# Kernel tuning notes

Measured on AMD Instinct MI355X. Metric: run time of the kernel, lower is better.

## Reference

```python
import jax, jax.numpy as jnp
import numpy as np

NF = 64   # num_feat
DG = 8    # deformable_groups (also conv groups)
B, H, W = 4, 96, 96
K = 9     # 3x3 kernel positions


def _conv(x, w, b, padding=1, dilation=1, groups=1):
    out = jax.lax.conv_general_dilated(
        x, w, (1, 1), [(padding, padding), (padding, padding)],
        rhs_dilation=(dilation, dilation),
        dimension_numbers=('NCHW', 'OIHW', 'NCHW'),
        feature_group_count=groups)
    return out + b[None, :, None, None]


def _lrelu(t):
    return jnp.where(t >= 0, t, 0.1 * t)


def _cat_align(a, b):
    # channel-interleaved concat: [a0,b0,a1,b1,...]
    Bn, k, h, w = a.shape
    return jnp.stack([a, b], axis=2).reshape(Bn, 2 * k, h, w)


def _deform_conv(x, offset, mask, weight, bias, dilation, padding):
    # DCNv2 modulated deformable conv, stride 1.
    Bn, C, h, w = x.shape
    Cpg = C // DG
    off = offset.reshape(Bn, DG, K, 2, h, w)          # (dy, dx) per group/kernel pos
    m = mask.reshape(Bn, DG, K, h, w)
    ky = (jnp.repeat(jnp.arange(3), 3) * dilation - padding).astype(x.dtype)  # (K,)
    kx = (jnp.tile(jnp.arange(3), 3) * dilation - padding).astype(x.dtype)
    hs = jnp.arange(h, dtype=x.dtype)
    ws = jnp.arange(w, dtype=x.dtype)
    py = off[:, :, :, 0] + ky[None, None, :, None, None] + hs[None, None, None, :, None]
    px = off[:, :, :, 1] + kx[None, None, :, None, None] + ws[None, None, None, None, :]
    y0f = jnp.floor(py); x0f = jnp.floor(px)
    ly = (py - y0f)[:, :, None]  # broadcast over Cpg
    lx = (px - x0f)[:, :, None]
    y0 = y0f.astype(jnp.int32); x0 = x0f.astype(jnp.int32)
    xg = x.reshape(Bn, DG, Cpg, h * w)

    def gather(yi, xi):
        inb = ((yi >= 0) & (yi < h) & (xi >= 0) & (xi < w))
        idx = (jnp.clip(yi, 0, h - 1) * w + jnp.clip(xi, 0, w - 1)).reshape(Bn, DG, 1, K * h * w)
        v = jnp.take_along_axis(xg, jnp.broadcast_to(idx, (Bn, DG, Cpg, K * h * w)), axis=3)
        return v.reshape(Bn, DG, Cpg, K, h, w) * inb[:, :, None].astype(x.dtype)

    v00 = gather(y0, x0); v01 = gather(y0, x0 + 1)
    v10 = gather(y0 + 1, x0); v11 = gather(y0 + 1, x0 + 1)
    val = (v00 * (1 - ly) * (1 - lx) + v01 * (1 - ly) * lx
           + v10 * ly * (1 - lx) + v11 * ly * lx) * m[:, :, None]
    sampled = val.reshape(Bn, C, K, h, w)
    out = jnp.einsum('bckhw,ock->bohw', sampled, weight.reshape(weight.shape[0], C, K))
    return out + bias[None, :, None, None]


def _dcn(x, off_feat, om_w, om_b, w, b, dilation):
    pad = dilation  # int(3/2)*dilation
    out = _conv(off_feat, om_w, om_b, padding=pad, dilation=dilation)
    o1, o2, msk = jnp.split(out, 3, axis=1)
    offset = jnp.concatenate([o1, o2], axis=1)
    mask = jax.nn.sigmoid(msk)
    return _deform_conv(x, offset, mask, w, b, dilation, pad)


def setup_inputs() -> dict:
    key = jax.random.key(0)
    ks = iter(jax.random.split(key, 64))
    def rn(shape, s=0.05):
        return jax.random.normal(next(ks), shape, jnp.float32) * s
    d = {}
    d['nbr_feat'] = jax.random.normal(next(ks), (B, NF, H, W), jnp.float32)
    d['ref_feat'] = jax.random.normal(next(ks), (B, NF, H, W), jnp.float32)
    for lv, has3 in [('l3', False), ('l2', True), ('l1', True)]:
        d[f'oc1_w_{lv}'] = rn((NF, 2 * NF // DG, 3, 3)); d[f'oc1_b_{lv}'] = rn((NF,))
        oc2_in = 2 * NF if has3 else NF
        d[f'oc2_w_{lv}'] = rn((NF, oc2_in // DG, 3, 3)); d[f'oc2_b_{lv}'] = rn((NF,))
        if has3:
            d[f'oc3_w_{lv}'] = rn((NF, NF // DG, 3, 3)); d[f'oc3_b_{lv}'] = rn((NF,))
            d[f'fc_w_{lv}'] = rn((NF, 2 * NF // DG, 3, 3)); d[f'fc_b_{lv}'] = rn((NF,))
        d[f'om_w_{lv}'] = rn((DG * 3 * K, NF, 3, 3), 0.01); d[f'om_b_{lv}'] = rn((DG * 3 * K,), 0.01)
        d[f'dcn_w_{lv}'] = rn((NF, NF, 3, 3)); d[f'dcn_b_{lv}'] = rn((NF,))
    d['cas_oc1_w'] = rn((NF, 2 * NF // DG, 3, 3)); d['cas_oc1_b'] = rn((NF,))
    d['cas_oc2_w'] = rn((NF, NF // DG, 3, 3)); d['cas_oc2_b'] = rn((NF,))
    d['cas_om_w'] = rn((DG * 3 * K, NF, 3, 3), 0.01); d['cas_om_b'] = rn((DG * 3 * K,), 0.01)
    d['cas_w'] = rn((NF, NF, 3, 3)); d['cas_b'] = rn((NF,))
    return d


def reference(nbr_feat, ref_feat,
              oc1_w_l3, oc1_b_l3, oc2_w_l3, oc2_b_l3, om_w_l3, om_b_l3, dcn_w_l3, dcn_b_l3,
              oc1_w_l2, oc1_b_l2, oc2_w_l2, oc2_b_l2, oc3_w_l2, oc3_b_l2, fc_w_l2, fc_b_l2,
              om_w_l2, om_b_l2, dcn_w_l2, dcn_b_l2,
              oc1_w_l1, oc1_b_l1, oc2_w_l1, oc2_b_l1, oc3_w_l1, oc3_b_l1, fc_w_l1, fc_b_l1,
              om_w_l1, om_b_l1, dcn_w_l1, dcn_b_l1,
              cas_oc1_w, cas_oc1_b, cas_oc2_w, cas_oc2_b, cas_om_w, cas_om_b, cas_w, cas_b):
    # level 3 (dilation 5)
    off = _lrelu(_conv(_cat_align(nbr_feat, ref_feat), oc1_w_l3, oc1_b_l3, groups=DG))
    off = _lrelu(_conv(off, oc2_w_l3, oc2_b_l3, groups=DG))
    feat = _lrelu(_dcn(nbr_feat, off, om_w_l3, om_b_l3, dcn_w_l3, dcn_b_l3, 5))
    to, tf = off, feat
    # level 2 (dilation 3)
    off = _lrelu(_conv(_cat_align(nbr_feat, ref_feat), oc1_w_l2, oc1_b_l2, groups=DG))
    off = _lrelu(_conv(_cat_align(off, to), oc2_w_l2, oc2_b_l2, groups=DG))
    off = _lrelu(_conv(off, oc3_w_l2, oc3_b_l2, groups=DG))
    feat = _dcn(nbr_feat, off, om_w_l2, om_b_l2, dcn_w_l2, dcn_b_l2, 3)
    feat = _lrelu(_conv(_cat_align(feat, tf), fc_w_l2, fc_b_l2, groups=DG))
    to, tf = off, feat
    # level 1 (dilation 1), no lrelu on feat
    off = _lrelu(_conv(_cat_align(nbr_feat, ref_feat), oc1_w_l1, oc1_b_l1, groups=DG))
    off = _lrelu(_conv(_cat_align(off, to), oc2_w_l1, oc2_b_l1, groups=DG))
    off = _lrelu(_conv(off, oc3_w_l1, oc3_b_l1, groups=DG))
    feat = _dcn(nbr_feat, off, om_w_l1, om_b_l1, dcn_w_l1, dcn_b_l1, 1)
    feat = _conv(_cat_align(feat, tf), fc_w_l1, fc_b_l1, groups=DG)
    # cascade
    off = _cat_align(feat, ref_feat)
    off = _lrelu(_conv(_lrelu(_conv(off, cas_oc1_w, cas_oc1_b, groups=DG)), cas_oc2_w, cas_oc2_b, groups=DG))
    feat = _lrelu(_dcn(feat, off, cas_om_w, cas_om_b, cas_w, cas_b, 1))
    return feat
```

## Files before the change

### kernel.cpp

```cpp
#include <hip/hip_runtime.h>

#define BATCH 4
#define NFEAT 64
#define DGRP 8
#define HH 96
#define WW 96
#define HWP (HH*WW)

typedef short short4a __attribute__((ext_vector_type(4)));
typedef short short8 __attribute__((ext_vector_type(8)));
typedef float f32x4 __attribute__((ext_vector_type(4)));
typedef float f32x16 __attribute__((ext_vector_type(16)));

__device__ inline short f2bf(float f) {
  union { float f; unsigned u; } v; v.f = f;
  unsigned r = v.u + 0x7fff + ((v.u >> 16) & 1);
  return (short)(r >> 16);
}
__device__ inline float bf2f(short s) {
  return __uint_as_float(((unsigned)(unsigned short)s) << 16);
}

__global__ __launch_bounds__(256) void prep_om(
    const float* __restrict__ s0, const float* __restrict__ s1,
    const float* __restrict__ s2, const float* __restrict__ s3,
    short* __restrict__ dst) {
  int gid = blockIdx.x * 256 + threadIdx.x;
  if (gid >= 4 * 147456) return;
  int t = gid / 147456, r = gid % 147456;
  int tile = r / 18432, r2 = r % 18432;
  int kk = r2 / 512, r3 = r2 % 512;
  int lane = r3 / 8, j = r3 % 8;
  int col = lane & 31, half = lane >> 5;
  int oc = tile * 32 + col;
  int k = kk * 16 + half * 8 + j;
  int p = k >> 6, c = k & 63;
  const float* s = (t == 0) ? s0 : (t == 1) ? s1 : (t == 2) ? s2 : s3;
  float v = (oc < 216) ? s[(size_t)oc * 576 + c * 9 + p] : 0.f;
  dst[gid] = f2bf(v);
}

__global__ __launch_bounds__(256) void prep_dcnw(
    const float* __restrict__ s0, const float* __restrict__ s1,
    const float* __restrict__ s2, const float* __restrict__ s3,
    short* __restrict__ dst) {
  int gid = blockIdx.x * 256 + threadIdx.x;
  if (gid >= 4 * 36864) return;
  int t = gid / 36864, r = gid % 36864;
  int tile = r / 18432, r2 = r % 18432;
  int kk = r2 / 512, r3 = r2 % 512;
  int lane = r3 / 8, j = r3 % 8;
  int col = lane & 31, half = lane >> 5;
  int oc = tile * 32 + col;
  int k = kk * 16 + half * 8 + j;
  int p = k >> 6, c = k & 63;
  const float* s = (t == 0) ? s0 : (t == 1) ? s1 : (t == 2) ? s2 : s3;
  dst[gid] = f2bf(s[(size_t)oc * 576 + c * 9 + p]);
}

struct GwArgs {
  const float* src[12];
  int cat[12];
  int base[13];
};

__global__ __launch_bounds__(256) void prep_gw(GwArgs a, short* __restrict__ dst) {
  int gid = blockIdx.x * 256 + threadIdx.x;
  if (gid >= a.base[12]) return;
  int t = 0;
  while (gid >= a.base[t + 1]) ++t;
  int r = gid - a.base[t];
  const float* s = a.src[t];
  const int tsz = a.cat[t] ? 4608 : 2560;
  int tile = r / tsz, r2 = r % tsz;
  int kk = r2 / 512, r3 = r2 % 512;
  int lane = r3 >> 3, j = r3 & 7;
  int m = lane & 15, quad = lane >> 4;
  int oc = tile * 16 + m;
  int j32 = quad * 8 + j;
  float val = 0.f;
  if (a.cat[t]) {
    int gsel = j32 >> 4, ssel = (j32 >> 3) & 1, ch8 = j32 & 7;
    if (gsel == (m >> 3)) val = s[oc * 144 + (2 * ch8 + ssel) * 9 + kk];
  } else {
    int tapsel = j32 >> 4, gsel = (j32 >> 3) & 1, ch8 = j32 & 7;
    int p = 2 * kk + tapsel;
    if (p < 9 && gsel == (m >> 3)) val = s[oc * 72 + ch8 * 9 + p];
  }
  dst[gid] = f2bf(val);
}

__global__ __launch_bounds__(256) void transpose_bf16(
    const float* __restrict__ in0, short* __restrict__ out0,
    const float* __restrict__ in1, short* __restrict__ out1) {
  const float* in = blockIdx.z ? in1 : in0;
  short* out = blockIdx.z ? out1 : out0;
  __shared__ float s[64][65];
  const int p0 = blockIdx.x * 64;
  const int b = blockIdx.y;
  const int tx = threadIdx.x, ty = threadIdx.y;
  for (int c = ty; c < 64; c += 4)
    s[c][tx] = in[((size_t)b * NFEAT + c) * HWP + p0 + tx];
  __syncthreads();
  for (int p = ty; p < 64; p += 4)
    out[((size_t)b * HWP + p0 + p) * NFEAT + tx] = f2bf(s[tx][p]);
}

template <bool CAT, bool LRELU>
__device__ __forceinline__ void gconv_body(
    const short* __restrict__ in0, const short* __restrict__ in1,
    const short* __restrict__ Wsh, const float* __restrict__ bias,
    short* __restrict__ out, int pixbase, int b) {
  const int lane = threadIdx.x, t = threadIdx.y;
  const int n = lane & 15, quad = lane >> 4;
  constexpr int NKK = CAT ? 9 : 5;

  short8 A[NKK];
#pragma unroll
  for (int kk = 0; kk < NKK; ++kk)
    A[kk] = *(const short8*)(Wsh + ((size_t)(t * NKK + kk) * 64 + lane) * 8);

  const short* sb;
  if (CAT) {
    sb = ((quad & 1) ? in1 : in0) + (size_t)b * HWP * 64 + (2 * t + (quad >> 1)) * 8;
  } else {
    sb = in0 + (size_t)b * HWP * 64 + (2 * t + (quad & 1)) * 8;
  }

  f32x4 acc[2] = {};
#pragma unroll
  for (int nt = 0; nt < 2; ++nt) {
    const int pix = pixbase + nt * 16 + n;
    const int yp = pix / WW, xp = pix % WW;
#pragma unroll
    for (int kk = 0; kk < NKK; ++kk) {
      const int p = CAT ? kk : (2 * kk + (quad >> 1));
      short8 B = {0, 0, 0, 0, 0, 0, 0, 0};
      if (p < 9) {
        const int sy = yp + p / 3 - 1, sx = xp + p % 3 - 1;
        if (((unsigned)sy < (unsigned)HH) && ((unsigned)sx < (unsigned)WW))
          B = *(const short8*)(sb + (size_t)(sy * WW + sx) * 64);
      }
      acc[nt] = __builtin_amdgcn_mfma_f32_16x16x32_bf16(A[kk], B, acc[nt], 0, 0, 0);
    }
  }

  const int ocb = t * 16 + quad * 4;
  const float b0 = bias[ocb], b1 = bias[ocb + 1], b2 = bias[ocb + 2], b3 = bias[ocb + 3];
#pragma unroll
  for (int nt = 0; nt < 2; ++nt) {
    float v0 = acc[nt][0] + b0, v1 = acc[nt][1] + b1;
    float v2 = acc[nt][2] + b2, v3 = acc[nt][3] + b3;
    if (LRELU) {
      v0 = (v0 >= 0.f) ? v0 : 0.1f * v0;
      v1 = (v1 >= 0.f) ? v1 : 0.1f * v1;
      v2 = (v2 >= 0.f) ? v2 : 0.1f * v2;
      v3 = (v3 >= 0.f) ? v3 : 0.1f * v3;
    }
    short4a pk = {f2bf(v0), f2bf(v1), f2bf(v2), f2bf(v3)};
    *(short4a*)(out + ((size_t)b * HWP + pixbase + nt * 16 + n) * 64 + ocb) = pk;
  }
}

template <bool CAT, bool LRELU>
__global__ __launch_bounds__(256) void gconv_mfma(
    const short* __restrict__ in0, const short* __restrict__ in1,
    const short* __restrict__ Wsh, const float* __restrict__ bias,
    short* __restrict__ out) {
  gconv_body<CAT, LRELU>(in0, in1, Wsh, bias, out, blockIdx.x * 32, blockIdx.y);
}

struct Oc1Args {
  const short* W[3];
  const float* bias[3];
  short* out[3];
};

__global__ __launch_bounds__(256) void gconv_oc1x3(
    const short* __restrict__ in0, const short* __restrict__ in1, Oc1Args a) {
  const int job = blockIdx.z;
  gconv_body<true, true>(in0, in1, a.W[job], a.bias[job], a.out[job],
                         blockIdx.x * 32, blockIdx.y);
}

#define OMPITCH 580
#define OMLP 33

template <int D, bool LRELU, bool PMOUT>
__global__ __launch_bounds__(256) void omdcn_fused(
    const short* __restrict__ omIn,
    const short* __restrict__ xT,
    const short* __restrict__ Wom,
    const float* __restrict__ obias,
    const short* __restrict__ Wd,
    const float* __restrict__ bias,
    void* __restrict__ outv) {
  __shared__ __align__(16) char smem[37120 + 14256];
  short* Bs = (short*)smem;
  short* Ls = (short*)smem;
  short* om_lds = (short*)(smem + 37120);
  float* red = (float*)(smem + 37120);

  const int tx = threadIdx.x, ty = threadIdx.y;
  const int lid = ty * 32 + tx;
  const int lane = lid & 63, w = lid >> 6;
  const int col = lane & 31, half = lane >> 5;
  const int pb = blockIdx.x, b = blockIdx.y;
  const int pixbase = pb * 32;

  {
    const short* pixb = omIn + (size_t)b * HWP * 64;
#pragma unroll
    for (int t = 0; t < 9; ++t) {
      const int i = lid + t * 256;
      const int row = i / 72, q = i % 72;
      const int p = q >> 3, c8 = q & 7;
      const int pix = pixbase + row;
      const int yp = pix / WW, xp = pix % WW;
      const int sy = yp + (p / 3 - 1) * D, sx = xp + (p % 3 - 1) * D;
      short4a lo = {0, 0, 0, 0}, hi = {0, 0, 0, 0};
      if (((unsigned)sy < (unsigned)HH) && ((unsigned)sx < (unsigned)WW)) {
        const short* src = pixb + (size_t)(sy * WW + sx) * 64 + c8 * 8;
        lo = *(const short4a*)src;
        hi = *(const short4a*)(src + 4);
      }
      short* dst = Bs + row * OMPITCH + q * 8;
      *(short4a*)dst = lo;
      *(short4a*)(dst + 4) = hi;
    }
  }
  __syncthreads();

  {
    const short* aP0 = Wom + ((size_t)(w * 36) * 64 + lane) * 8;
    const short* aP1 = Wom + ((size_t)((w + 4) * 36) * 64 + lane) * 8;
    const short* bbase = Bs + col * OMPITCH + half * 8;
    f32x16 acc0 = {}, acc1 = {};
#pragma unroll 4
    for (int kk = 0; kk < 36; ++kk) {
      const short* bp = bbase + kk * 16;
      short4a l = *(const short4a*)bp, h = *(const short4a*)(bp + 4);
      short8 B = {l[0], l[1], l[2], l[3], h[0], h[1], h[2], h[3]};
      short8 A0 = *(const short8*)(aP0 + (size_t)kk * 512);
      short8 A1 = *(const short8*)(aP1 + (size_t)kk * 512);
      acc0 = __builtin_amdgcn_mfma_f32_32x32x16_bf16(A0, B, acc0, 0, 0, 0);
      acc1 = __builtin_amdgcn_mfma_f32_32x32x16_bf16(A1, B, acc1, 0, 0, 0);
    }
#pragma unroll
    for (int r = 0; r < 16; ++r) {
      const int rrow = (r & 3) + 8 * (r >> 2) + 4 * half;
      const int oc0 = w * 32 + rrow;
      om_lds[oc0 * OMLP + col] = f2bf(acc0[r] + obias[oc0]);
      const int oc1 = (w + 4) * 32 + rrow;
      if (oc1 < 216)
        om_lds[oc1 * OMLP + col] = f2bf(acc1[r] + obias[oc1]);
    }
  }
  __syncthreads();

  {
    const int px = tx, dg = ty;
    const int pix = pixbase + px;
    const int yp = pix / WW, xp = pix % WW;
    const short* xb = xT + (size_t)b * HWP * 64 + dg * 8;
    short* Sp = Ls + (size_t)((dg & 1) * 32 + px) * 8;

#pragma unroll
    for (int k = 0; k < 9; ++k) {
      float dy = bf2f(om_lds[(dg * 18 + 2 * k) * OMLP + px]);
      float dxv = bf2f(om_lds[(dg * 18 + 2 * k + 1) * OMLP + px]);
      float mr = bf2f(om_lds[(144 + dg * 9 + k) * OMLP + px]);
      float m = 1.f / (1.f + __expf(-mr));
      float py = (float)(yp + (k / 3 - 1) * D) + dy;
      float px_ = (float)(xp + (k % 3 - 1) * D) + dxv;
      float y0f = floorf(py), x0f = floorf(px_);
      float ly = py - y0f, lx = px_ - x0f;
      int y0 = (int)y0f, x0 = (int)x0f;
      int y1 = y0 + 1, x1 = x0 + 1;
      bool vy0 = (unsigned)y0 < (unsigned)HH, vy1 = (unsigned)y1 < (unsigned)HH;
      bool vx0 = (unsigned)x0 < (unsigned)WW, vx1 = (unsigned)x1 < (unsigned)WW;
      int cy0 = min(max(y0, 0), HH - 1), cy1 = min(max(y1, 0), HH - 1);
      int cx0 = min(max(x0, 0), WW - 1), cx1 = min(max(x1, 0), WW - 1);
      float w00 = (vy0 && vx0) ? (1.f - ly) * (1.f - lx) * m : 0.f;
      float w01 = (vy0 && vx1) ? (1.f - ly) * lx * m : 0.f;
      float w10 = (vy1 && vx0) ? ly * (1.f - lx) * m : 0.f;
      float w11 = (vy1 && vx1) ? ly * lx * m : 0.f;
      short8 s00 = *(const short8*)(xb + (size_t)(cy0 * WW + cx0) * 64);
      short8 s01 = *(const short8*)(xb + (size_t)(cy0 * WW + cx1) * 64);
      short8 s10 = *(const short8*)(xb + (size_t)(cy1 * WW + cx0) * 64);
      short8 s11 = *(const short8*)(xb + (size_t)(cy1 * WW + cx1) * 64);
      short8 pk;
#pragma unroll
      for (int cl = 0; cl < 8; ++cl) {
        float v = w00 * bf2f(s00[cl]) + w01 * bf2f(s01[cl]) +
                  w10 * bf2f(s10[cl]) + w11 * bf2f(s11[cl]);
        pk[cl] = f2bf(v);
      }
      const int kk = k * 4 + (dg >> 1);
      *(short8*)(Sp + (size_t)kk * 512) = pk;
    }
  }
  __syncthreads();

  const int octile = w & 1, kh = w >> 1;
  const int pix = pixbase + col;

  const short* aP = Wd + ((size_t)(octile * 36) * 64 + lane) * 8;
  const short* bP = Ls + (size_t)lane * 8;

  f32x16 acc = {};
#pragma unroll 6
  for (int kk = 0; kk < 18; ++kk) {
    const int kkg = kh * 18 + kk;
    short8 A = *(const short8*)(aP + (size_t)kkg * 512);
    short8 B = *(const short8*)(bP + (size_t)kkg * 512);
    acc = __builtin_amdgcn_mfma_f32_32x32x16_bf16(A, B, acc, 0, 0, 0);
  }

  if (kh == 1) {
#pragma unroll
    for (int r = 0; r < 16; ++r) red[(octile * 64 + lane) * 17 + r] = acc[r];
  }
  __syncthreads();
  if (kh == 0) {
    if (PMOUT) {
      short* out = (short*)outv;
#pragma unroll
      for (int rg = 0; rg < 4; ++rg) {
        short4a pk;
#pragma unroll
        for (int i = 0; i < 4; ++i) {
          const int r = rg * 4 + i;
          const int oc = octile * 32 + i + 8 * rg + 4 * half;
          float v = acc[r] + red[(octile * 64 + lane) * 17 + r] + bias[oc];
          if (LRELU) v = (v >= 0.f) ? v : 0.1f * v;
          pk[i] = f2bf(v);
        }
        *(short4a*)(out + ((size_t)b * HWP + pix) * 64 + octile * 32 + 8 * rg + 4 * half) = pk;
      }
    } else {
      float* out = (float*)outv;
#pragma unroll
      for (int r = 0; r < 16; ++r) {
        const int oc = octile * 32 + (r & 3) + 8 * (r >> 2) + 4 * half;
        float v = acc[r] + red[(octile * 64 + lane) * 17 + r] + bias[oc];
        if (LRELU) v = (v >= 0.f) ? v : 0.1f * v;
        out[((size_t)b * NFEAT + oc) * HWP + pix] = v;
      }
    }
  }
}

extern "C" void kernel_launch(void* const* d_in, const int* in_sizes, int n_in,
                              void* d_out, int out_size, void* d_ws, size_t ws_size,
                              hipStream_t stream) {
  const float* nbr = (const float*)d_in[0];
  const float* ref = (const float*)d_in[1];
  auto f = [&](int i) { return (const float*)d_in[i]; };

  short* s0 = (short*)d_ws;
  const size_t PM = (size_t)BATCH * HWP * 64;
  short* omB = s0;
  short* refT = omB + 7962624;
  short* pmA = refT + PM;
  short* pmB = pmA + PM;
  short* pmC = pmB + PM;
  short* pmD = pmC + PM;
  short* pmE = pmD + PM;
  short* pmF = pmE + PM;
  short* pmG = pmF + PM;
  short* wbf = pmG + PM;
  short* wdcn = wbf + 589824;
  short* wgc = wdcn + 147456;
  short* nbrT = (short*)d_out;

  prep_om<<<(4 * 147456 + 255) / 256, 256, 0, stream>>>(f(6), f(18), f(30), f(38), wbf);
  prep_dcnw<<<(4 * 36864 + 255) / 256, 256, 0, stream>>>(f(8), f(20), f(32), f(40), wdcn);

  static const int gSrc[12] = {2, 4, 10, 12, 14, 16, 22, 24, 26, 28, 34, 36};
  static const int gCat[12] = {1, 0, 1, 1, 0, 1, 1, 1, 0, 1, 1, 0};
  GwArgs ga;
  int gb = 0;
  const short* wg[12];
  for (int t = 0; t < 12; ++t) {
    ga.src[t] = f(gSrc[t]);
    ga.cat[t] = gCat[t];
    ga.base[t] = gb;
    wg[t] = wgc + gb;
    gb += gCat[t] ? 18432 : 10240;
  }
  ga.base[12] = gb;
  prep_gw<<<(gb + 255) / 256, 256, 0, stream>>>(ga, wgc);

  short* wbf_l3 = wbf;
  short* wbf_l2 = wbf + 147456;
  short* wbf_l1 = wbf + 2 * 147456;
  short* wbf_cas = wbf + 3 * 147456;
  short* wd_l3 = wdcn;
  short* wd_l2 = wdcn + 36864;
  short* wd_l1 = wdcn + 2 * 36864;
  short* wd_cas = wdcn + 3 * 36864;

  dim3 gcGrid(288, BATCH), gcBlk(64, 4);
  dim3 oc1Grid(288, BATCH, 3);
  dim3 fGrid(288, BATCH), fBlk(32, 8);
  dim3 trGrid(HWP / 64, BATCH, 2), trBlk(64, 4);

  transpose_bf16<<<trGrid, trBlk, 0, stream>>>(nbr, nbrT, ref, refT);

  Oc1Args oa;
  oa.W[0] = wg[0]; oa.bias[0] = f(3);  oa.out[0] = pmA;
  oa.W[1] = wg[2]; oa.bias[1] = f(11); oa.out[1] = pmF;
  oa.W[2] = wg[6]; oa.bias[2] = f(23); oa.out[2] = pmG;
  gconv_oc1x3<<<oc1Grid, gcBlk, 0, stream>>>(nbrT, refT, oa);

  gconv_mfma<false, true><<<gcGrid, gcBlk, 0, stream>>>(pmA, nullptr, wg[1], f(5), pmB);
  omdcn_fused<5, true, true><<<fGrid, fBlk, 0, stream>>>(
      pmB, nbrT, wbf_l3, f(7), wd_l3, f(9), pmC);

  gconv_mfma<true, true><<<gcGrid, gcBlk, 0, stream>>>(pmF, pmB, wg[3], f(13), pmD);
  gconv_mfma<false, true><<<gcGrid, gcBlk, 0, stream>>>(pmD, nullptr, wg[4], f(15), pmE);
  omdcn_fused<3, false, true><<<fGrid, fBlk, 0, stream>>>(
      pmE, nbrT, wbf_l2, f(19), wd_l2, f(21), pmD);
  gconv_mfma<true, true><<<gcGrid, gcBlk, 0, stream>>>(pmD, pmC, wg[5], f(17), pmA);

  gconv_mfma<true, true><<<gcGrid, gcBlk, 0, stream>>>(pmG, pmE, wg[7], f(25), pmB);
  gconv_mfma<false, true><<<gcGrid, gcBlk, 0, stream>>>(pmB, nullptr, wg[8], f(27), pmC);
  omdcn_fused<1, false, true><<<fGrid, fBlk, 0, stream>>>(
      pmC, nbrT, wbf_l1, f(31), wd_l1, f(33), pmD);
  gconv_mfma<true, false><<<gcGrid, gcBlk, 0, stream>>>(pmD, pmA, wg[9], f(29), pmB);

  gconv_mfma<true, true><<<gcGrid, gcBlk, 0, stream>>>(pmB, refT, wg[10], f(35), pmC);
  gconv_mfma<false, true><<<gcGrid, gcBlk, 0, stream>>>(pmC, nullptr, wg[11], f(37), pmD);
  omdcn_fused<1, true, false><<<fGrid, fBlk, 0, stream>>>(
      pmD, pmB, wbf_cas, f(39), wd_cas, f(41), (float*)d_out);
}
```

Measured before the change: 546.1 us.

## Load offset-conv B operands from global directly and split DCN sampling into halves

The offset/mask conv in the fused DCN kernel now reads its im2col B fragments straight from global memory into registers, instead of first staging them in a padded LDS buffer and syncing. The deformable sampling buffer is halved: samples for kernel positions 0-4 are written, consumed by MFMA, then overwritten by positions 4-8. LDS per block drops from about 51KB to about 32KB, which is meant to raise occupancy and remove a staging pass. In exchange it adds extra barriers, replaces coalesced staged loads with scattered per-lane global loads, and removes the LDS row padding (pitch 33 to 32), which may cause bank conflicts.

```diff
diff --git a/kernel.cpp b/kernel.cpp
--- a/kernel.cpp
+++ b/kernel.cpp
@@ -183,9 +183,6 @@
                          blockIdx.x * 32, blockIdx.y);
 }
 
-#define OMPITCH 580
-#define OMLP 33
-
 template <int D, bool LRELU, bool PMOUT>
 __global__ __launch_bounds__(256) void omdcn_fused(
     const short* __restrict__ omIn,
@@ -195,11 +192,10 @@
     const short* __restrict__ Wd,
     const float* __restrict__ bias,
     void* __restrict__ outv) {
-  __shared__ __align__(16) char smem[37120 + 14256];
-  short* Bs = (short*)smem;
+  __shared__ __align__(16) char smem[18432 + 13824];
   short* Ls = (short*)smem;
-  short* om_lds = (short*)(smem + 37120);
-  float* red = (float*)(smem + 37120);
+  short* om_lds = (short*)(smem + 18432);
+  float* red = (float*)(smem + 18432);
 
   const int tx = threadIdx.x, ty = threadIdx.y;
   const int lid = ty * 32 + tx;
@@ -210,116 +206,114 @@
 
   {
     const short* pixb = omIn + (size_t)b * HWP * 64;
-#pragma unroll
-    for (int t = 0; t < 9; ++t) {
-      const int i = lid + t * 256;
-      const int row = i / 72, q = i % 72;
-      const int p = q >> 3, c8 = q & 7;
-      const int pix = pixbase + row;
-      const int yp = pix / WW, xp = pix % WW;
-      const int sy = yp + (p / 3 - 1) * D, sx = xp + (p % 3 - 1) * D;
-      short4a lo = {0, 0, 0, 0}, hi = {0, 0, 0, 0};
-      if (((unsigned)sy < (unsigned)HH) && ((unsigned)sx < (unsigned)WW)) {
-        const short* src = pixb + (size_t)(sy * WW + sx) * 64 + c8 * 8;
-        lo = *(const short4a*)src;
-        hi = *(const short4a*)(src + 4);
-      }
-      short* dst = Bs + row * OMPITCH + q * 8;
-      *(short4a*)dst = lo;
-      *(short4a*)(dst + 4) = hi;
-    }
-  }
-  __syncthreads();
-
-  {
     const short* aP0 = Wom + ((size_t)(w * 36) * 64 + lane) * 8;
     const short* aP1 = Wom + ((size_t)((w + 4) * 36) * 64 + lane) * 8;
-    const short* bbase = Bs + col * OMPITCH + half * 8;
+    const int pix = pixbase + col;
+    const int yp = pix / WW, xp = pix % WW;
     f32x16 acc0 = {}, acc1 = {};
-#pragma unroll 4
-    for (int kk = 0; kk < 36; ++kk) {
-      const short* bp = bbase + kk * 16;
-      short4a l = *(const short4a*)bp, h = *(const short4a*)(bp + 4);
-      short8 B = {l[0], l[1], l[2], l[3], h[0], h[1], h[2], h[3]};
-      short8 A0 = *(const short8*)(aP0 + (size_t)kk * 512);
-      short8 A1 = *(const short8*)(aP1 + (size_t)kk * 512);
-      acc0 = __builtin_amdgcn_mfma_f32_32x32x16_bf16(A0, B, acc0, 0, 0, 0);
-      acc1 = __builtin_amdgcn_mfma_f32_32x32x16_bf16(A1, B, acc1, 0, 0, 0);
+#pragma unroll
+    for (int p = 0; p < 9; ++p) {
+      const int sy = yp + (p / 3 - 1) * D, sx = xp + (p % 3 - 1) * D;
+      const bool valid = ((unsigned)sy < (unsigned)HH) && ((unsigned)sx < (unsigned)WW);
+      const short* bsrc = pixb + (size_t)(sy * WW + sx) * 64 + half * 8;
+#pragma unroll
+      for (int q = 0; q < 4; ++q) {
+        const int kk = p * 4 + q;
+        short8 B = {0, 0, 0, 0, 0, 0, 0, 0};
+        if (valid) B = *(const short8*)(bsrc + q * 16);
+        short8 A0 = *(const short8*)(aP0 + (size_t)kk * 512);
+        short8 A1 = *(const short8*)(aP1 + (size_t)kk * 512);
+        acc0 = __builtin_amdgcn_mfma_f32_32x32x16_bf16(A0, B, acc0, 0, 0, 0);
+        acc1 = __builtin_amdgcn_mfma_f32_32x32x16_bf16(A1, B, acc1, 0, 0, 0);
+      }
     }
 #pragma unroll
     for (int r = 0; r < 16; ++r) {
       const int rrow = (r & 3) + 8 * (r >> 2) + 4 * half;
       const int oc0 = w * 32 + rrow;
-      om_lds[oc0 * OMLP + col] = f2bf(acc0[r] + obias[oc0]);
+      om_lds[oc0 * 32 + col] = f2bf(acc0[r] + obias[oc0]);
       const int oc1 = (w + 4) * 32 + rrow;
       if (oc1 < 216)
-        om_lds[oc1 * OMLP + col] = f2bf(acc1[r] + obias[oc1]);
-    }
-  }
-  __syncthreads();
-
-  {
-    const int px = tx, dg = ty;
-    const int pix = pixbase + px;
-    const int yp = pix / WW, xp = pix % WW;
-    const short* xb = xT + (size_t)b * HWP * 64 + dg * 8;
-    short* Sp = Ls + (size_t)((dg & 1) * 32 + px) * 8;
-
-#pragma unroll
-    for (int k = 0; k < 9; ++k) {
-      float dy = bf2f(om_lds[(dg * 18 + 2 * k) * OMLP + px]);
-      float dxv = bf2f(om_lds[(dg * 18 + 2 * k + 1) * OMLP + px]);
-      float mr = bf2f(om_lds[(144 + dg * 9 + k) * OMLP + px]);
-      float m = 1.f / (1.f + __expf(-mr));
-      float py = (float)(yp + (k / 3 - 1) * D) + dy;
-      float px_ = (float)(xp + (k % 3 - 1) * D) + dxv;
-      float y0f = floorf(py), x0f = floorf(px_);
-      float ly = py - y0f, lx = px_ - x0f;
-      int y0 = (int)y0f, x0 = (int)x0f;
-      int y1 = y0 + 1, x1 = x0 + 1;
-      bool vy0 = (unsigned)y0 < (unsigned)HH, vy1 = (unsigned)y1 < (unsigned)HH;
-      bool vx0 = (unsigned)x0 < (unsigned)WW, vx1 = (unsigned)x1 < (unsigned)WW;
-      int cy0 = min(max(y0, 0), HH - 1), cy1 = min(max(y1, 0), HH - 1);
-      int cx0 = min(max(x0, 0), WW - 1), cx1 = min(max(x1, 0), WW - 1);
-      float w00 = (vy0 && vx0) ? (1.f - ly) * (1.f - lx) * m : 0.f;
-      float w01 = (vy0 && vx1) ? (1.f - ly) * lx * m : 0.f;
-      float w10 = (vy1 && vx0) ? ly * (1.f - lx) * m : 0.f;
-      float w11 = (vy1 && vx1) ? ly * lx * m : 0.f;
-      short8 s00 = *(const short8*)(xb + (size_t)(cy0 * WW + cx0) * 64);
-      short8 s01 = *(const short8*)(xb + (size_t)(cy0 * WW + cx1) * 64);
-      short8 s10 = *(const short8*)(xb + (size_t)(cy1 * WW + cx0) * 64);
-      short8 s11 = *(const short8*)(xb + (size_t)(cy1 * WW + cx1) * 64);
-      short8 pk;
-#pragma unroll
-      for (int cl = 0; cl < 8; ++cl) {
-        float v = w00 * bf2f(s00[cl]) + w01 * bf2f(s01[cl]) +
-                  w10 * bf2f(s10[cl]) + w11 * bf2f(s11[cl]);
-        pk[cl] = f2bf(v);
-      }
-      const int kk = k * 4 + (dg >> 1);
-      *(short8*)(Sp + (size_t)kk * 512) = pk;
-    }
-  }
-  __syncthreads();
+        om_lds[oc1 * 32 + col] = f2bf(acc1[r] + obias[oc1]);
+    }
+  }
+  __syncthreads();
+
+  const int dg = ty;
+  const int pixS = pixbase + tx;
+  const int ypS = pixS / WW, xpS = pixS % WW;
+  const short* xb = xT + (size_t)b * HWP * 64 + dg * 8;
+  short* Sp = Ls + (size_t)((dg & 1) * 32 + tx) * 8;
+
+  auto sample_k = [&](int k, int slotbase) {
+    float dy = bf2f(om_lds[(dg * 18 + 2 * k) * 32 + tx]);
+    float dxv = bf2f(om_lds[(dg * 18 + 2 * k + 1) * 32 + tx]);
+    float mr = bf2f(om_lds[(144 + dg * 9 + k) * 32 + tx]);
+    float m = 1.f / (1.f + __expf(-mr));
+    float py = (float)(ypS + (k / 3 - 1) * D) + dy;
+    float px_ = (float)(xpS + (k % 3 - 1) * D) + dxv;
+    float y0f = floorf(py), x0f = floorf(px_);
+    float ly = py - y0f, lx = px_ - x0f;
+    int y0 = (int)y0f, x0 = (int)x0f;
+    int y1 = y0 + 1, x1 = x0 + 1;
+    bool vy0 = (unsigned)y0 < (unsigned)HH, vy1 = (unsigned)y1 < (unsigned)HH;
+    bool vx0 = (unsigned)x0 < (unsigned)WW, vx1 = (unsigned)x1 < (unsigned)WW;
+    int cy0 = min(max(y0, 0), HH - 1), cy1 = min(max(y1, 0), HH - 1);
+    int cx0 = min(max(x0, 0), WW - 1), cx1 = min(max(x1, 0), WW - 1);
+    float w00 = (vy0 && vx0) ? (1.f - ly) * (1.f - lx) * m : 0.f;
+    float w01 = (vy0 && vx1) ? (1.f - ly) * lx * m : 0.f;
+    float w10 = (vy1 && vx0) ? ly * (1.f - lx) * m : 0.f;
+    float w11 = (vy1 && vx1) ? ly * lx * m : 0.f;
+    short8 s00 = *(const short8*)(xb + (size_t)(cy0 * WW + cx0) * 64);
+    short8 s01 = *(const short8*)(xb + (size_t)(cy0 * WW + cx1) * 64);
+    short8 s10 = *(const short8*)(xb + (size_t)(cy1 * WW + cx0) * 64);
+    short8 s11 = *(const short8*)(xb + (size_t)(cy1 * WW + cx1) * 64);
+    short8 pk;
+#pragma unroll
+    for (int cl = 0; cl < 8; ++cl) {
+      float v = w00 * bf2f(s00[cl]) + w01 * bf2f(s01[cl]) +
+                w10 * bf2f(s10[cl]) + w11 * bf2f(s11[cl]);
+      pk[cl] = f2bf(v);
+    }
+    const int slot = k * 4 + (dg >> 1) - slotbase;
+    *(short8*)(Sp + (size_t)slot * 512) = pk;
+  };
 
   const int octile = w & 1, kh = w >> 1;
+  const short* aPd = Wd + ((size_t)(octile * 36) * 64 + lane) * 8;
+  const short* bPd = Ls + (size_t)lane * 8;
+  f32x16 accd = {};
+
+#pragma unroll
+  for (int k = 0; k < 4; ++k) sample_k(k, 0);
+  if (dg < 4) sample_k(4, 0);
+  __syncthreads();
+#pragma unroll
+  for (int i = 0; i < 9; ++i) {
+    const int kkg = kh * 9 + i;
+    short8 A = *(const short8*)(aPd + (size_t)kkg * 512);
+    short8 B = *(const short8*)(bPd + (size_t)kkg * 512);
+    accd = __builtin_amdgcn_mfma_f32_32x32x16_bf16(A, B, accd, 0, 0, 0);
+  }
+  __syncthreads();
+
+  if (dg >= 4) sample_k(4, 18);
+#pragma unroll
+  for (int k = 5; k < 9; ++k) sample_k(k, 18);
+  __syncthreads();
+#pragma unroll
+  for (int i = 0; i < 9; ++i) {
+    const int kkg = 18 + kh * 9 + i;
+    const int kkl = kh * 9 + i;
+    short8 A = *(const short8*)(aPd + (size_t)kkg * 512);
+    short8 B = *(const short8*)(bPd + (size_t)kkl * 512);
+    accd = __builtin_amdgcn_mfma_f32_32x32x16_bf16(A, B, accd, 0, 0, 0);
+  }
+
   const int pix = pixbase + col;
-
-  const short* aP = Wd + ((size_t)(octile * 36) * 64 + lane) * 8;
-  const short* bP = Ls + (size_t)lane * 8;
-
-  f32x16 acc = {};
-#pragma unroll 6
-  for (int kk = 0; kk < 18; ++kk) {
-    const int kkg = kh * 18 + kk;
-    short8 A = *(const short8*)(aP + (size_t)kkg * 512);
-    short8 B = *(const short8*)(bP + (size_t)kkg * 512);
-    acc = __builtin_amdgcn_mfma_f32_32x32x16_bf16(A, B, acc, 0, 0, 0);
-  }
-
   if (kh == 1) {
 #pragma unroll
-    for (int r = 0; r < 16; ++r) red[(octile * 64 + lane) * 17 + r] = acc[r];
+    for (int r = 0; r < 16; ++r) red[(octile * 64 + lane) * 17 + r] = accd[r];
   }
   __syncthreads();
   if (kh == 0) {
@@ -332,7 +326,7 @@
         for (int i = 0; i < 4; ++i) {
           const int r = rg * 4 + i;
           const int oc = octile * 32 + i + 8 * rg + 4 * half;
-          float v = acc[r] + red[(octile * 64 + lane) * 17 + r] + bias[oc];
+          float v = accd[r] + red[(octile * 64 + lane) * 17 + r] + bias[oc];
           if (LRELU) v = (v >= 0.f) ? v : 0.1f * v;
           pk[i] = f2bf(v);
         }
@@ -343,7 +337,7 @@
 #pragma unroll
       for (int r = 0; r < 16; ++r) {
         const int oc = octile * 32 + (r & 3) + 8 * (r >> 2) + 4 * half;
-        float v = acc[r] + red[(octile * 64 + lane) * 17 + r] + bias[oc];
+        float v = accd[r] + red[(octile * 64 + lane) * 17 + r] + bias[oc];
         if (LRELU) v = (v >= 0.f) ? v : 0.1f * v;
         out[((size_t)b * NFEAT + oc) * HWP + pix] = v;
       }
```

Result: slower. 581.2 us (+6.4%).
